# Kernel optimization log

Hardware: AMD Instinct MI355X
Metric: run time of the kernel (lower is better)

The kernel has to match this reference:

```python
import jax, jax.numpy as jnp
import numpy as np

OBS_DIM = 768; H = 128; W = 128
OBJ_DIM = 128; REL_DIM = 64; N_SLOTS = 32; ACT_DIM = 16; HID = 256
EPS = 1e-8; DT = 0.1; N_ITERS = 3
REND_IN = OBJ_DIM * N_SLOTS + REL_DIM * N_SLOTS * N_SLOTS  # 69632


def _ln(x, g, b):
    m = x.mean(-1, keepdims=True)
    v = ((x - m) ** 2).mean(-1, keepdims=True)
    return (x - m) / jnp.sqrt(v + 1e-5) * g + b


def setup_inputs() -> dict:
    key = jax.random.key(0)
    ks = iter(jax.random.split(key, 48))

    def w(shape):
        fan = shape[-2] if len(shape) > 1 else shape[0]
        return jax.random.normal(next(ks), shape, jnp.float32) / np.sqrt(fan)

    d = {}
    d['obs'] = jax.random.normal(next(ks), (1, H, W, OBS_DIM), jnp.float32)
    d['action'] = jax.random.normal(next(ks), (1, ACT_DIM), jnp.float32)
    d['slot_noise'] = jax.random.normal(next(ks), (1, N_SLOTS, OBJ_DIM), jnp.float32)
    d['slots_mu'] = jax.random.normal(next(ks), (1, 1, OBJ_DIM), jnp.float32)
    d['slots_log_sigma'] = jax.random.normal(next(ks), (1, 1, OBJ_DIM), jnp.float32) * 0.1 - 1.0
    d['ln_in_g'] = jnp.ones((OBS_DIM,)); d['ln_in_b'] = jnp.zeros((OBS_DIM,))
    d['ln_s_g'] = jnp.ones((OBJ_DIM,)); d['ln_s_b'] = jnp.zeros((OBJ_DIM,))
    d['ln_m_g'] = jnp.ones((OBJ_DIM,)); d['ln_m_b'] = jnp.zeros((OBJ_DIM,))
    d['Wq'] = w((OBJ_DIM, OBJ_DIM)); d['Wk'] = w((OBS_DIM, OBJ_DIM)); d['Wv'] = w((OBS_DIM, OBJ_DIM))
    d['mlp_w1'] = w((OBJ_DIM, 2 * OBJ_DIM)); d['mlp_b1'] = jnp.zeros((2 * OBJ_DIM,))
    d['mlp_w2'] = w((2 * OBJ_DIM, OBJ_DIM)); d['mlp_b2'] = jnp.zeros((OBJ_DIM,))
    d['prop_w1'] = w((OBJ_DIM, HID)); d['prop_b1'] = jnp.zeros((HID,))
    d['prop_w2'] = w((HID, OBJ_DIM)); d['prop_b2'] = jnp.zeros((OBJ_DIM,))
    d['rel_w1'] = w((2 * OBJ_DIM, 2 * REL_DIM)); d['rel_b1'] = jnp.zeros((2 * REL_DIM,))
    d['rel_w2'] = w((2 * REL_DIM, REL_DIM)); d['rel_b2'] = jnp.zeros((REL_DIM,))
    d['dyn_w1'] = w((OBJ_DIM + ACT_DIM, HID)); d['dyn_b1'] = jnp.zeros((HID,))
    d['dyn_w2'] = w((HID, HID)); d['dyn_b2'] = jnp.zeros((HID,))
    d['dyn_w3'] = w((HID, OBJ_DIM)); d['dyn_b3'] = jnp.zeros((OBJ_DIM,))
    d['gravity'] = jnp.array([0.0, -9.8, 0.0], jnp.float32)
    d['rend_w1'] = w((REND_IN, 2 * OBS_DIM)); d['rend_b1'] = jnp.zeros((2 * OBS_DIM,))
    d['rend_w2'] = w((2 * OBS_DIM, OBS_DIM)); d['rend_b2'] = jnp.zeros((OBS_DIM,))
    return d


def reference(obs, action, slot_noise, slots_mu, slots_log_sigma,
              ln_in_g, ln_in_b, ln_s_g, ln_s_b, ln_m_g, ln_m_b,
              Wq, Wk, Wv, mlp_w1, mlp_b1, mlp_w2, mlp_b2,
              prop_w1, prop_b1, prop_w2, prop_b2,
              rel_w1, rel_b1, rel_w2, rel_b2,
              dyn_w1, dyn_b1, dyn_w2, dyn_b2, dyn_w3, dyn_b3,
              gravity, rend_w1, rend_b1, rend_w2, rend_b2):
    B = obs.shape[0]
    # --- slot attention over flattened feature map ---
    x = obs.reshape(B, -1, OBS_DIM)                 # [B, HW, C]
    x = _ln(x, ln_in_g, ln_in_b)
    k = x @ Wk                                      # [B, HW, D]
    v = x @ Wv                                      # [B, HW, D]
    slots = slots_mu + jnp.exp(slots_log_sigma) * slot_noise  # [B, S, D]
    scale = OBJ_DIM ** -0.5
    for _ in range(N_ITERS):
        prev = slots
        q = _ln(slots, ln_s_g, ln_s_b) @ Wq
        logits = jnp.einsum('bsd,bnd->bsn', q, k) * scale
        attn = jax.nn.softmax(logits, axis=1)       # softmax over slots (dim=1)
        attn = attn / (attn.sum(-1, keepdims=True) + EPS)
        slots = prev + jnp.einsum('bsn,bnd->bsd', attn, v)
        h = _ln(slots, ln_m_g, ln_m_b)
        slots = slots + (jax.nn.relu(h @ mlp_w1 + mlp_b1) @ mlp_w2 + mlp_b2)
    # --- object property decoding ---
    objects = jax.nn.relu(slots @ prop_w1 + prop_b1) @ prop_w2 + prop_b2  # [B, S, D]
    # --- pairwise relation encoding (O(S^2)) ---
    S = N_SLOTS
    oi = jnp.broadcast_to(objects[:, :, None, :], (B, S, S, OBJ_DIM))
    oj = jnp.broadcast_to(objects[:, None, :, :], (B, S, S, OBJ_DIM))
    pairs = jnp.concatenate([oi, oj], -1)            # [B, S, S, 2D]
    relations = jax.nn.relu(pairs @ rel_w1 + rel_b1) @ rel_w2 + rel_b2  # [B, S, S, REL]
    # --- scene graph takes batch element 0 (as in torch source) ---
    obj0 = objects[0:1]                              # [1, S, D]
    rel0 = relations[0]                              # [S, S, REL]
    # --- physics engine ---
    a = jnp.broadcast_to(action[:, None, :], (1, S, ACT_DIM))
    inp = jnp.concatenate([obj0, a], -1)
    h = jax.nn.relu(inp @ dyn_w1 + dyn_b1)
    h = jax.nn.relu(h @ dyn_w2 + dyn_b2)
    delta = h @ dyn_w3 + dyn_b3                      # [1, S, D]
    delta = delta.at[:, :, :3].add(gravity * DT)
    next_objects = obj0 + delta * DT                 # [1, S, D]
    # --- render next observation ---
    feat = jnp.concatenate([next_objects.reshape(1, -1), rel0.reshape(1, -1)], -1)
    next_obs = jax.nn.relu(feat @ rend_w1 + rend_b1) @ rend_w2 + rend_b2  # [1, OBS_DIM]
    return next_obs
```

## Files before the change

kernel.cpp:

```cpp
#include <hip/hip_runtime.h>
#include <hip/hip_bf16.h>
#include <math.h>

#define NPIX    16384
#define OBSD    768
#define OBJ     128
#define NS      32
#define HIDD    256
#define RELD    64
#define ACTD    16
#define QSCALE  0.08838834764831845f
#define LNEPS   1e-5f
#define ATEPS   1e-8f
#define DTC     0.1f

#define OFF_STATS 0
#define OFF_KV    (OFF_STATS + NPIX*2)
#define OFF_SLOTS (OFF_KV + NPIX*256)
#define OFF_Q     (OFF_SLOTS + 4096)
#define OFF_H     (OFF_Q + 4096)
#define OFF_APART (OFF_H + 4096)
#define OFF_OBJ   (OFF_APART + 256*4128)
#define OFF_FEAT  (OFF_OBJ + 4096)
#define OFF_P1    (OFF_FEAT + 69632)
#define OFF_HREND (OFF_P1 + 1024*1536)
#define OFF_P3    (OFF_HREND + 1536)

__global__ __launch_bounds__(256) void k_stats_initq(
    const float* __restrict__ obs, float* __restrict__ stats,
    const float* __restrict__ mu, const float* __restrict__ lsig,
    const float* __restrict__ noise, float* __restrict__ slots,
    const float* __restrict__ Wq,
    const float* __restrict__ g, const float* __restrict__ b,
    float* __restrict__ qg)
{
    __shared__ float red[256];
    __shared__ float hh[128];
    int t = threadIdx.x;
    if (blockIdx.x < 4096) {
        int lane = t & 63;
        int w    = t >> 6;
        int row  = blockIdx.x * 4 + w;
        const float* o = obs + (size_t)row * OBSD;
        float s = 0.f, s2 = 0.f;
        #pragma unroll
        for (int i = 0; i < 12; ++i) { float v = o[lane + 64*i]; s += v; s2 += v*v; }
        #pragma unroll
        for (int off = 32; off > 0; off >>= 1) {
            s  += __shfl_down(s,  off);
            s2 += __shfl_down(s2, off);
        }
        if (lane == 0) {
            float m   = s  * (1.f/OBSD);
            float var = s2 * (1.f/OBSD) - m*m;
            stats[row*2]   = m;
            stats[row*2+1] = rsqrtf(var + LNEPS);
        }
        return;
    }
    int s = blockIdx.x - 4096;
    int d = t & 127, half = t >> 7;
    float x = 0.f;
    if (t < 128) {
        x = mu[t] + expf(lsig[t]) * noise[s*128 + t];
        slots[s*128 + t] = x;
    }
    red[t] = (t < 128) ? x : 0.f;
    __syncthreads();
    #pragma unroll
    for (int off = 128; off > 0; off >>= 1) { if (t < off) red[t] += red[t+off]; __syncthreads(); }
    float mean = red[0] * (1.f/128.f);
    __syncthreads();
    { float dx = (t < 128) ? (x - mean) : 0.f; red[t] = dx*dx; }
    __syncthreads();
    #pragma unroll
    for (int off = 128; off > 0; off >>= 1) { if (t < off) red[t] += red[t+off]; __syncthreads(); }
    float rstd = rsqrtf(red[0] * (1.f/128.f) + LNEPS);
    __syncthreads();
    if (t < 128) hh[t] = (x - mean) * rstd * g[t] + b[t];
    __syncthreads();
    float acc = 0.f;
    for (int c = half*64; c < half*64 + 64; ++c) acc = fmaf(hh[c], Wq[c*128 + d], acc);
    red[t] = acc;
    __syncthreads();
    if (t < 128) qg[s*128 + t] = red[t] + red[t+128];
}

#define STA 129
__global__ __launch_bounds__(256) void k_kv(
    const float* __restrict__ obs, const float* __restrict__ stats,
    const float* __restrict__ g, const float* __restrict__ b,
    const float* __restrict__ Wk, const float* __restrict__ Wv,
    float* __restrict__ kv)
{
    __shared__ float As[32*STA];
    __shared__ float Bs[32*128];
    __shared__ float sm[128], sr[128];
    int t  = threadIdx.x;
    int m0 = blockIdx.x * 128;
    int nsel = blockIdx.y;
    const float* W = nsel ? Wv : Wk;
    int tx = t & 15, ty = t >> 4;
    float acc[8][8];
    #pragma unroll
    for (int i = 0; i < 8; ++i) {
        #pragma unroll
        for (int j = 0; j < 8; ++j) acc[i][j] = 0.f;
    }
    if (t < 128) { sm[t] = stats[(m0+t)*2]; sr[t] = stats[(m0+t)*2+1]; }

    for (int ks = 0; ks < 24; ++ks) {
        int k0 = ks * 32;
        __syncthreads();
        #pragma unroll
        for (int r = 0; r < 16; ++r) {
            int id = t + 256*r;
            int m  = id >> 5, kk = id & 31;
            float val = obs[(size_t)(m0+m)*OBSD + k0 + kk];
            val = (val - sm[m]) * sr[m] * g[k0+kk] + b[k0+kk];
            As[kk*STA + m] = val;
        }
        #pragma unroll
        for (int r = 0; r < 16; ++r) {
            int id = t + 256*r;
            int kk = id >> 7, jj = id & 127;
            Bs[kk*128 + jj] = W[(size_t)(k0+kk)*128 + jj];
        }
        __syncthreads();
        #pragma unroll
        for (int kk = 0; kk < 32; ++kk) {
            float a8[8], b8[8];
            #pragma unroll
            for (int i = 0; i < 8; ++i) a8[i] = As[kk*STA + ty*8 + i];
            float4 u0 = *(const float4*)&Bs[kk*128 + tx*8];
            float4 u1 = *(const float4*)&Bs[kk*128 + tx*8 + 4];
            b8[0]=u0.x; b8[1]=u0.y; b8[2]=u0.z; b8[3]=u0.w;
            b8[4]=u1.x; b8[5]=u1.y; b8[6]=u1.z; b8[7]=u1.w;
            #pragma unroll
            for (int i = 0; i < 8; ++i) {
                #pragma unroll
                for (int j = 0; j < 8; ++j)
                    acc[i][j] = fmaf(a8[i], b8[j], acc[i][j]);
            }
        }
    }
    #pragma unroll
    for (int i = 0; i < 8; ++i) {
        size_t row = (size_t)(m0 + ty*8 + i);
        float4 o0 = make_float4(acc[i][0], acc[i][1], acc[i][2], acc[i][3]);
        float4 o1 = make_float4(acc[i][4], acc[i][5], acc[i][6], acc[i][7]);
        *(float4*)&kv[row*256 + nsel*128 + tx*8]     = o0;
        *(float4*)&kv[row*256 + nsel*128 + tx*8 + 4] = o1;
    }
}

#define STK 129
#define STQ 132
#define STT 36
__global__ __launch_bounds__(256) void k_attn(
    const float* __restrict__ kv, const float* __restrict__ qg,
    float* __restrict__ part)
{
    __shared__ float q_lds[NS*STQ];
    __shared__ float k_lds[64*STK];
    __shared__ float at[64*STT];
    int t   = threadIdx.x;
    int px0 = blockIdx.x * 64;
    #pragma unroll
    for (int r = 0; r < 16; ++r) {
        int id = t + 256*r;
        int s = id >> 7, d = id & 127;
        q_lds[s*STQ + d] = qg[id];
    }
    #pragma unroll
    for (int r = 0; r < 32; ++r) {
        int id = t + 256*r;
        int p = id >> 7, d = id & 127;
        k_lds[p*STK + d] = kv[(size_t)(px0+p)*256 + d];
    }
    __syncthreads();

    int wv = t >> 6, p = t & 63;
    float acc[8];
    #pragma unroll
    for (int u = 0; u < 8; ++u) acc[u] = 0.f;
    for (int dc = 0; dc < 4; ++dc) {
        float kr[32];
        #pragma unroll
        for (int d = 0; d < 32; ++d) kr[d] = k_lds[p*STK + dc*32 + d];
        #pragma unroll
        for (int u = 0; u < 8; ++u) {
            int s = u*4 + wv;
            const float* qp = &q_lds[s*STQ + dc*32];
            #pragma unroll
            for (int ii = 0; ii < 8; ++ii) {
                float4 q4 = *(const float4*)(qp + 4*ii);
                acc[u] = fmaf(q4.x, kr[4*ii+0], acc[u]);
                acc[u] = fmaf(q4.y, kr[4*ii+1], acc[u]);
                acc[u] = fmaf(q4.z, kr[4*ii+2], acc[u]);
                acc[u] = fmaf(q4.w, kr[4*ii+3], acc[u]);
            }
        }
    }
    #pragma unroll
    for (int u = 0; u < 8; ++u) at[p*STT + u*4 + wv] = acc[u] * QSCALE;
    __syncthreads();

    if (t < 64) {
        float mx = -1e30f;
        #pragma unroll
        for (int s = 0; s < NS; ++s) mx = fmaxf(mx, at[t*STT + s]);
        float smv = 0.f;
        #pragma unroll
        for (int s = 0; s < NS; ++s) { float e = expf(at[t*STT + s] - mx); at[t*STT + s] = e; smv += e; }
        float inv = 1.f / smv;
        #pragma unroll
        for (int s = 0; s < NS; ++s) at[t*STT + s] *= inv;
    }
    __syncthreads();

    int d = t & 127, sh = t >> 7;
    float u16[16];
    #pragma unroll
    for (int i = 0; i < 16; ++i) u16[i] = 0.f;
    const float* vbase = kv + (size_t)px0*256 + 128 + d;
    #pragma unroll 4
    for (int pp = 0; pp < 64; ++pp) {
        float vv = vbase[(size_t)pp*256];
        const float4* ap = (const float4*)&at[pp*STT + sh*16];
        #pragma unroll
        for (int gg = 0; gg < 4; ++gg) {
            float4 a4 = ap[gg];
            u16[4*gg+0] = fmaf(a4.x, vv, u16[4*gg+0]);
            u16[4*gg+1] = fmaf(a4.y, vv, u16[4*gg+1]);
            u16[4*gg+2] = fmaf(a4.z, vv, u16[4*gg+2]);
            u16[4*gg+3] = fmaf(a4.w, vv, u16[4*gg+3]);
        }
    }
    float* P = part + (size_t)blockIdx.x * 4128;
    #pragma unroll
    for (int g2 = 0; g2 < 16; ++g2) P[(sh*16 + g2)*128 + d] = u16[g2];
    if (t < 32) {
        float ss = 0.f;
        for (int pp = 0; pp < 64; ++pp) ss += at[pp*STT + t];
        P[4096 + t] = ss;
    }
}

__global__ __launch_bounds__(256) void k_umq(
    const float* __restrict__ part, float* __restrict__ slots,
    const float* __restrict__ gm, const float* __restrict__ bm,
    const float* __restrict__ w1, const float* __restrict__ b1,
    const float* __restrict__ w2, const float* __restrict__ b2,
    const float* __restrict__ gs, const float* __restrict__ bs,
    const float* __restrict__ Wq, float* __restrict__ qg,
    const float* __restrict__ pw1, const float* __restrict__ pb1,
    const float* __restrict__ pw2, const float* __restrict__ pb2,
    const float* __restrict__ action,
    const float* __restrict__ dw1, const float* __restrict__ db1,
    const float* __restrict__ dw2, const float* __restrict__ db2,
    const float* __restrict__ dw3, const float* __restrict__ db3,
    const float* __restrict__ gravity,
    float* __restrict__ objects, float* __restrict__ feat, int last)
{
    int s = blockIdx.x, t = threadIdx.x;
    int d = t & 127, half = t >> 7;
    __shared__ float red[256];
    __shared__ float ssred[2];
    __shared__ float xs[128], hm[128], hid[256];
    __shared__ float inp[144], h2[256];

    float u = 0.f, ss = 0.f;
    const float* P0 = part + (size_t)(half * 128) * 4128;
    for (int bb = 0; bb < 128; ++bb) {
        const float* P = P0 + (size_t)bb * 4128;
        u  += P[s*128 + d];
        ss += P[4096 + s];
    }
    red[t] = u;
    if (d == 0) ssred[half] = ss;
    __syncthreads();
    if (half == 0)
        xs[d] = slots[s*128 + d] + (red[d] + red[d+128]) / (ssred[0] + ssred[1] + ATEPS);
    __syncthreads();

    red[t] = (half == 0) ? xs[d] : 0.f;
    __syncthreads();
    #pragma unroll
    for (int off = 128; off > 0; off >>= 1) { if (t < off) red[t] += red[t+off]; __syncthreads(); }
    float mean = red[0] * (1.f/128.f);
    __syncthreads();
    { float dx = (half == 0) ? (xs[d] - mean) : 0.f; red[t] = dx*dx; }
    __syncthreads();
    #pragma unroll
    for (int off = 128; off > 0; off >>= 1) { if (t < off) red[t] += red[t+off]; __syncthreads(); }
    float rstd = rsqrtf(red[0] * (1.f/128.f) + LNEPS);
    __syncthreads();
    if (half == 0) hm[d] = (xs[d] - mean) * rstd * gm[d] + bm[d];
    __syncthreads();

    float a = b1[t];
    for (int c = 0; c < 128; ++c) a = fmaf(hm[c], w1[c*256 + t], a);
    hid[t] = fmaxf(a, 0.f);
    __syncthreads();
    if (half == 0) {
        float o = b2[d];
        for (int j = 0; j < 256; ++j) o = fmaf(hid[j], w2[j*128 + d], o);
        float xn = xs[d] + o;
        slots[s*128 + d] = xn;
        xs[d] = xn;
    }
    __syncthreads();

    if (!last) {
        red[t] = (half == 0) ? xs[d] : 0.f;
        __syncthreads();
        #pragma unroll
        for (int off = 128; off > 0; off >>= 1) { if (t < off) red[t] += red[t+off]; __syncthreads(); }
        float m2 = red[0] * (1.f/128.f);
        __syncthreads();
        { float dx = (half == 0) ? (xs[d] - m2) : 0.f; red[t] = dx*dx; }
        __syncthreads();
        #pragma unroll
        for (int off = 128; off > 0; off >>= 1) { if (t < off) red[t] += red[t+off]; __syncthreads(); }
        float r2 = rsqrtf(red[0] * (1.f/128.f) + LNEPS);
        __syncthreads();
        if (half == 0) hm[d] = (xs[d] - m2) * r2 * gs[d] + bs[d];
        __syncthreads();
        float acc = 0.f;
        for (int c = half*64; c < half*64 + 64; ++c) acc = fmaf(hm[c], Wq[c*128 + d], acc);
        red[t] = acc;
        __syncthreads();
        if (half == 0) qg[s*128 + d] = red[d] + red[d+128];
    } else {
        float a1 = pb1[t];
        for (int c = 0; c < 128; ++c) a1 = fmaf(xs[c], pw1[c*256 + t], a1);
        hid[t] = fmaxf(a1, 0.f);
        __syncthreads();
        if (t < 128) {
            float o = pb2[t];
            for (int j = 0; j < 256; ++j) o = fmaf(hid[j], pw2[j*128 + t], o);
            objects[s*128 + t] = o;
            inp[t] = o;
        } else if (t < 144) {
            inp[t] = action[t - 128];
        }
        __syncthreads();
        float a2 = db1[t];
        for (int c = 0; c < 144; ++c) a2 = fmaf(inp[c], dw1[c*256 + t], a2);
        hid[t] = fmaxf(a2, 0.f);
        __syncthreads();
        float a3 = db2[t];
        for (int c = 0; c < 256; ++c) a3 = fmaf(hid[c], dw2[c*256 + t], a3);
        h2[t] = fmaxf(a3, 0.f);
        __syncthreads();
        if (t < 128) {
            float dlt = db3[t];
            for (int c = 0; c < 256; ++c) dlt = fmaf(h2[c], dw3[c*128 + t], dlt);
            if (t < 3) dlt += gravity[t] * DTC;
            feat[s*128 + t] = inp[t] + dlt * DTC;
        }
    }
}

__global__ __launch_bounds__(128) void k_rel(
    const float* __restrict__ objects, const float* __restrict__ w1, const float* __restrict__ b1,
    const float* __restrict__ w2, const float* __restrict__ b2, float* __restrict__ rel_out)
{
    int pr = blockIdx.x; int i = pr >> 5, j = pr & 31; int t = threadIdx.x;
    __shared__ float pair[256], hid[128];
    pair[t]       = objects[i*128 + t];
    pair[128 + t] = objects[j*128 + t];
    __syncthreads();
    float a = b1[t];
    for (int c = 0; c < 256; ++c) a = fmaf(pair[c], w1[c*128 + t], a);
    hid[t] = fmaxf(a, 0.f);
    __syncthreads();
    if (t < 64) {
        float o = b2[t];
        for (int c = 0; c < 128; ++c) o = fmaf(hid[c], w2[c*64 + t], o);
        rel_out[(size_t)pr*64 + t] = o;
    }
}

__global__ __launch_bounds__(384) void k_rend1(
    const float* __restrict__ feat, const float* __restrict__ w1, float* __restrict__ p1)
{
    int b = blockIdx.x, t = threadIdx.x;
    float4 acc = make_float4(0.f, 0.f, 0.f, 0.f);
    int i0 = b * 68;
    #pragma unroll 4
    for (int r = 0; r < 68; ++r) {
        int i = i0 + r;
        float f = feat[i];
        float4 w = *(const float4*)(w1 + (size_t)i * 1536 + 4*t);
        acc.x = fmaf(f, w.x, acc.x);
        acc.y = fmaf(f, w.y, acc.y);
        acc.z = fmaf(f, w.z, acc.z);
        acc.w = fmaf(f, w.w, acc.w);
    }
    *(float4*)(p1 + (size_t)b * 1536 + 4*t) = acc;
}

__global__ __launch_bounds__(256) void k_rend23(
    const float* __restrict__ p1, const float* __restrict__ b1,
    const float* __restrict__ w2, float* __restrict__ p3)
{
    int bj = blockIdx.x, t = threadIdx.x;
    int j0 = bj * 32;
    int tj = t & 31, tr = t >> 5;
    __shared__ float red2[256];
    __shared__ float hh[32];
    float part = 0.f;
    const float* P = p1 + (size_t)tr * 1536 + j0 + tj;
    #pragma unroll 8
    for (int r = 0; r < 128; ++r) part += P[(size_t)r * 8 * 1536];
    red2[t] = part;
    __syncthreads();
    if (t < 32) {
        float a = b1[j0 + t];
        #pragma unroll
        for (int g = 0; g < 8; ++g) a += red2[g*32 + t];
        hh[t] = fmaxf(a, 0.f);
    }
    __syncthreads();
    float a0 = 0.f, a1 = 0.f, a2 = 0.f;
    #pragma unroll
    for (int j = 0; j < 32; ++j) {
        float hj = hh[j];
        const float* w = w2 + (size_t)(j0 + j) * 768;
        a0 = fmaf(hj, w[t],       a0);
        a1 = fmaf(hj, w[t + 256], a1);
        a2 = fmaf(hj, w[t + 512], a2);
    }
    p3[(size_t)bj*768 + t]       = a0;
    p3[(size_t)bj*768 + t + 256] = a1;
    p3[(size_t)bj*768 + t + 512] = a2;
}

__global__ __launch_bounds__(256) void k_rend4(
    const float* __restrict__ p3, const float* __restrict__ b2, float* __restrict__ out)
{
    int m = blockIdx.x * 256 + threadIdx.x;
    float a = b2[m];
    #pragma unroll
    for (int bj = 0; bj < 48; ++bj) a += p3[(size_t)bj*768 + m];
    out[m] = a;
}

extern "C" void kernel_launch(void* const* d_in, const int* in_sizes, int n_in,
                              void* d_out, int out_size, void* d_ws, size_t ws_size,
                              hipStream_t stream) {
    (void)in_sizes; (void)n_in; (void)out_size; (void)ws_size;
    const float* obs      = (const float*)d_in[0];
    const float* action   = (const float*)d_in[1];
    const float* noise    = (const float*)d_in[2];
    const float* mu       = (const float*)d_in[3];
    const float* lsig     = (const float*)d_in[4];
    const float* ln_in_g  = (const float*)d_in[5];
    const float* ln_in_b  = (const float*)d_in[6];
    const float* ln_s_g   = (const float*)d_in[7];
    const float* ln_s_b   = (const float*)d_in[8];
    const float* ln_m_g   = (const float*)d_in[9];
    const float* ln_m_b   = (const float*)d_in[10];
    const float* Wq       = (const float*)d_in[11];
    const float* Wk       = (const float*)d_in[12];
    const float* Wv       = (const float*)d_in[13];
    const float* mlp_w1   = (const float*)d_in[14];
    const float* mlp_b1   = (const float*)d_in[15];
    const float* mlp_w2   = (const float*)d_in[16];
    const float* mlp_b2   = (const float*)d_in[17];
    const float* prop_w1  = (const float*)d_in[18];
    const float* prop_b1  = (const float*)d_in[19];
    const float* prop_w2  = (const float*)d_in[20];
    const float* prop_b2  = (const float*)d_in[21];
    const float* rel_w1   = (const float*)d_in[22];
    const float* rel_b1   = (const float*)d_in[23];
    const float* rel_w2   = (const float*)d_in[24];
    const float* rel_b2   = (const float*)d_in[25];
    const float* dyn_w1   = (const float*)d_in[26];
    const float* dyn_b1   = (const float*)d_in[27];
    const float* dyn_w2   = (const float*)d_in[28];
    const float* dyn_b2   = (const float*)d_in[29];
    const float* dyn_w3   = (const float*)d_in[30];
    const float* dyn_b3   = (const float*)d_in[31];
    const float* gravity  = (const float*)d_in[32];
    const float* rend_w1  = (const float*)d_in[33];
    const float* rend_b1  = (const float*)d_in[34];
    const float* rend_w2  = (const float*)d_in[35];
    const float* rend_b2  = (const float*)d_in[36];
    float* out = (float*)d_out;

    float* w      = (float*)d_ws;
    float* stats  = w + OFF_STATS;
    float* kv     = w + OFF_KV;
    float* slots  = w + OFF_SLOTS;
    float* qg     = w + OFF_Q;
    float* apart  = w + OFF_APART;
    float* objs   = w + OFF_OBJ;
    float* feat   = w + OFF_FEAT;
    float* relout = feat + 4096;
    float* p1     = w + OFF_P1;
    float* p3     = w + OFF_P3;

    k_stats_initq<<<4128, 256, 0, stream>>>(obs, stats, mu, lsig, noise, slots,
                                            Wq, ln_s_g, ln_s_b, qg);
    k_kv<<<dim3(128, 2), 256, 0, stream>>>(obs, stats, ln_in_g, ln_in_b, Wk, Wv, kv);

    for (int it = 0; it < 3; ++it) {
        k_attn<<<256, 256, 0, stream>>>(kv, qg, apart);
        k_umq<<<32, 256, 0, stream>>>(apart, slots, ln_m_g, ln_m_b,
                                      mlp_w1, mlp_b1, mlp_w2, mlp_b2,
                                      ln_s_g, ln_s_b, Wq, qg,
                                      prop_w1, prop_b1, prop_w2, prop_b2,
                                      action, dyn_w1, dyn_b1, dyn_w2, dyn_b2,
                                      dyn_w3, dyn_b3, gravity,
                                      objs, feat, (it == 2) ? 1 : 0);
    }

    k_rel<<<1024, 128, 0, stream>>>(objs, rel_w1, rel_b1, rel_w2, rel_b2, relout);

    k_rend1<<<1024, 384, 0, stream>>>(feat, rend_w1, p1);
    k_rend23<<<48, 256, 0, stream>>>(p1, rend_b1, rend_w2, p3);
    k_rend4<<<3, 256, 0, stream>>>(p3, rend_b2, out);
}
```

Baseline: 985.2 us.

## Fuse slot-attention iterations and relation MLP into persistent kernel with grid barrier

Replaces the six alternating attention/update kernel launches and the relation kernel with one persistent 256-block kernel. Phases are separated by a software sense-reversing grid barrier built on atomics. The goal is to remove launch gaps and tail effects between the small dependent kernels. In exchange it needs all 256 blocks co-resident to avoid deadlock, idles most blocks during the 32-block update phase, and pays atomic spin-wait costs at each barrier.

```diff
diff --git a/kernel.cpp b/kernel.cpp
--- a/kernel.cpp
+++ b/kernel.cpp
@@ -25,6 +25,7 @@
 #define OFF_P1    (OFF_FEAT + 69632)
 #define OFF_HREND (OFF_P1 + 1024*1536)
 #define OFF_P3    (OFF_HREND + 1536)
+#define OFF_BAR   (OFF_P3 + 48*768)
 
 __global__ __launch_bounds__(256) void k_stats_initq(
     const float* __restrict__ obs, float* __restrict__ stats,
@@ -32,7 +33,7 @@
     const float* __restrict__ noise, float* __restrict__ slots,
     const float* __restrict__ Wq,
     const float* __restrict__ g, const float* __restrict__ b,
-    float* __restrict__ qg)
+    float* __restrict__ qg, int* __restrict__ bar)
 {
     __shared__ float red[256];
     __shared__ float hh[128];
@@ -59,6 +60,7 @@
         return;
     }
     int s = blockIdx.x - 4096;
+    if (s == 0 && t < 2) bar[t] = 0;
     int d = t & 127, half = t >> 7;
     float x = 0.f;
     if (t < 128) {
@@ -154,232 +156,255 @@
     }
 }
 
+__device__ __forceinline__ void gbar(int* cnt, int* sense, int nblk, int want)
+{
+    __syncthreads();
+    if (threadIdx.x == 0) {
+        __threadfence();
+        int prev = atomicAdd(cnt, 1);
+        if (prev == nblk - 1) {
+            atomicExch(cnt, 0);
+            __threadfence();
+            atomicExch(sense, want);
+        } else {
+            while (atomicAdd(sense, 0) != want)
+                __builtin_amdgcn_s_sleep(2);
+            __threadfence();
+        }
+    }
+    __syncthreads();
+}
+
 #define STK 129
 #define STQ 132
 #define STT 36
-__global__ __launch_bounds__(256) void k_attn(
-    const float* __restrict__ kv, const float* __restrict__ qg,
-    float* __restrict__ part)
-{
-    __shared__ float q_lds[NS*STQ];
-    __shared__ float k_lds[64*STK];
-    __shared__ float at[64*STT];
+
+struct SLArgs {
+    const float* kv;
+    const float* gs; const float* bs; const float* Wq;
+    const float* gm; const float* bm;
+    const float* w1; const float* b1; const float* w2; const float* b2;
+    const float* pw1; const float* pb1; const float* pw2; const float* pb2;
+    const float* action;
+    const float* dw1; const float* db1; const float* dw2; const float* db2;
+    const float* dw3; const float* db3; const float* gravity;
+    const float* rw1; const float* rb1; const float* rw2; const float* rb2;
+    float* slots; float* qg; float* part; float* objects; float* feat; float* relout;
+    int* bcnt; int* bsen;
+};
+
+__global__ __launch_bounds__(256) void k_mega(SLArgs a)
+{
+    __shared__ union {
+        struct { float q[NS*STQ]; float k[64*STK]; float at[64*STT]; } A;
+        struct { float red[256]; float ssred[2]; float xs[128]; float hm[128];
+                 float hid[256]; float inp[144]; float h2[256]; } U;
+        struct { float pair[2][256]; float hid[2][128]; } R;
+    } sm;
     int t   = threadIdx.x;
-    int px0 = blockIdx.x * 64;
-    #pragma unroll
-    for (int r = 0; r < 16; ++r) {
-        int id = t + 256*r;
-        int s = id >> 7, d = id & 127;
-        q_lds[s*STQ + d] = qg[id];
-    }
-    #pragma unroll
-    for (int r = 0; r < 32; ++r) {
-        int id = t + 256*r;
-        int p = id >> 7, d = id & 127;
-        k_lds[p*STK + d] = kv[(size_t)(px0+p)*256 + d];
-    }
-    __syncthreads();
-
-    int wv = t >> 6, p = t & 63;
-    float acc[8];
-    #pragma unroll
-    for (int u = 0; u < 8; ++u) acc[u] = 0.f;
-    for (int dc = 0; dc < 4; ++dc) {
-        float kr[32];
-        #pragma unroll
-        for (int d = 0; d < 32; ++d) kr[d] = k_lds[p*STK + dc*32 + d];
-        #pragma unroll
-        for (int u = 0; u < 8; ++u) {
-            int s = u*4 + wv;
-            const float* qp = &q_lds[s*STQ + dc*32];
-            #pragma unroll
-            for (int ii = 0; ii < 8; ++ii) {
-                float4 q4 = *(const float4*)(qp + 4*ii);
-                acc[u] = fmaf(q4.x, kr[4*ii+0], acc[u]);
-                acc[u] = fmaf(q4.y, kr[4*ii+1], acc[u]);
-                acc[u] = fmaf(q4.z, kr[4*ii+2], acc[u]);
-                acc[u] = fmaf(q4.w, kr[4*ii+3], acc[u]);
-            }
-        }
-    }
-    #pragma unroll
-    for (int u = 0; u < 8; ++u) at[p*STT + u*4 + wv] = acc[u] * QSCALE;
-    __syncthreads();
-
-    if (t < 64) {
-        float mx = -1e30f;
-        #pragma unroll
-        for (int s = 0; s < NS; ++s) mx = fmaxf(mx, at[t*STT + s]);
-        float smv = 0.f;
-        #pragma unroll
-        for (int s = 0; s < NS; ++s) { float e = expf(at[t*STT + s] - mx); at[t*STT + s] = e; smv += e; }
-        float inv = 1.f / smv;
-        #pragma unroll
-        for (int s = 0; s < NS; ++s) at[t*STT + s] *= inv;
-    }
-    __syncthreads();
-
-    int d = t & 127, sh = t >> 7;
-    float u16[16];
-    #pragma unroll
-    for (int i = 0; i < 16; ++i) u16[i] = 0.f;
-    const float* vbase = kv + (size_t)px0*256 + 128 + d;
-    #pragma unroll 4
-    for (int pp = 0; pp < 64; ++pp) {
-        float vv = vbase[(size_t)pp*256];
-        const float4* ap = (const float4*)&at[pp*STT + sh*16];
-        #pragma unroll
-        for (int gg = 0; gg < 4; ++gg) {
-            float4 a4 = ap[gg];
-            u16[4*gg+0] = fmaf(a4.x, vv, u16[4*gg+0]);
-            u16[4*gg+1] = fmaf(a4.y, vv, u16[4*gg+1]);
-            u16[4*gg+2] = fmaf(a4.z, vv, u16[4*gg+2]);
-            u16[4*gg+3] = fmaf(a4.w, vv, u16[4*gg+3]);
-        }
-    }
-    float* P = part + (size_t)blockIdx.x * 4128;
-    #pragma unroll
-    for (int g2 = 0; g2 < 16; ++g2) P[(sh*16 + g2)*128 + d] = u16[g2];
-    if (t < 32) {
-        float ss = 0.f;
-        for (int pp = 0; pp < 64; ++pp) ss += at[pp*STT + t];
-        P[4096 + t] = ss;
-    }
-}
-
-__global__ __launch_bounds__(256) void k_umq(
-    const float* __restrict__ part, float* __restrict__ slots,
-    const float* __restrict__ gm, const float* __restrict__ bm,
-    const float* __restrict__ w1, const float* __restrict__ b1,
-    const float* __restrict__ w2, const float* __restrict__ b2,
-    const float* __restrict__ gs, const float* __restrict__ bs,
-    const float* __restrict__ Wq, float* __restrict__ qg,
-    const float* __restrict__ pw1, const float* __restrict__ pb1,
-    const float* __restrict__ pw2, const float* __restrict__ pb2,
-    const float* __restrict__ action,
-    const float* __restrict__ dw1, const float* __restrict__ db1,
-    const float* __restrict__ dw2, const float* __restrict__ db2,
-    const float* __restrict__ dw3, const float* __restrict__ db3,
-    const float* __restrict__ gravity,
-    float* __restrict__ objects, float* __restrict__ feat, int last)
-{
-    int s = blockIdx.x, t = threadIdx.x;
+    int blk = blockIdx.x;
     int d = t & 127, half = t >> 7;
-    __shared__ float red[256];
-    __shared__ float ssred[2];
-    __shared__ float xs[128], hm[128], hid[256];
-    __shared__ float inp[144], h2[256];
-
-    float u = 0.f, ss = 0.f;
-    const float* P0 = part + (size_t)(half * 128) * 4128;
-    for (int bb = 0; bb < 128; ++bb) {
-        const float* P = P0 + (size_t)bb * 4128;
-        u  += P[s*128 + d];
-        ss += P[4096 + s];
-    }
-    red[t] = u;
-    if (d == 0) ssred[half] = ss;
-    __syncthreads();
-    if (half == 0)
-        xs[d] = slots[s*128 + d] + (red[d] + red[d+128]) / (ssred[0] + ssred[1] + ATEPS);
-    __syncthreads();
-
-    red[t] = (half == 0) ? xs[d] : 0.f;
-    __syncthreads();
-    #pragma unroll
-    for (int off = 128; off > 0; off >>= 1) { if (t < off) red[t] += red[t+off]; __syncthreads(); }
-    float mean = red[0] * (1.f/128.f);
-    __syncthreads();
-    { float dx = (half == 0) ? (xs[d] - mean) : 0.f; red[t] = dx*dx; }
-    __syncthreads();
-    #pragma unroll
-    for (int off = 128; off > 0; off >>= 1) { if (t < off) red[t] += red[t+off]; __syncthreads(); }
-    float rstd = rsqrtf(red[0] * (1.f/128.f) + LNEPS);
-    __syncthreads();
-    if (half == 0) hm[d] = (xs[d] - mean) * rstd * gm[d] + bm[d];
-    __syncthreads();
-
-    float a = b1[t];
-    for (int c = 0; c < 128; ++c) a = fmaf(hm[c], w1[c*256 + t], a);
-    hid[t] = fmaxf(a, 0.f);
-    __syncthreads();
-    if (half == 0) {
-        float o = b2[d];
-        for (int j = 0; j < 256; ++j) o = fmaf(hid[j], w2[j*128 + d], o);
-        float xn = xs[d] + o;
-        slots[s*128 + d] = xn;
-        xs[d] = xn;
-    }
-    __syncthreads();
-
-    if (!last) {
-        red[t] = (half == 0) ? xs[d] : 0.f;
+    int ls = 0;
+
+    for (int it = 0; it < 3; ++it) {
+        {
+            int px0 = blk * 64;
+            __syncthreads();
+            #pragma unroll
+            for (int r = 0; r < 16; ++r) {
+                int id = t + 256*r;
+                int s2 = id >> 7, dd = id & 127;
+                sm.A.q[s2*STQ + dd] = a.qg[id];
+            }
+            #pragma unroll
+            for (int r = 0; r < 32; ++r) {
+                int id = t + 256*r;
+                int p = id >> 7, dd = id & 127;
+                sm.A.k[p*STK + dd] = a.kv[(size_t)(px0+p)*256 + dd];
+            }
+            __syncthreads();
+
+            int wv = t >> 6, p = t & 63;
+            float acc[8];
+            #pragma unroll
+            for (int u = 0; u < 8; ++u) acc[u] = 0.f;
+            for (int dc = 0; dc < 4; ++dc) {
+                float kr[32];
+                #pragma unroll
+                for (int dd = 0; dd < 32; ++dd) kr[dd] = sm.A.k[p*STK + dc*32 + dd];
+                #pragma unroll
+                for (int u = 0; u < 8; ++u) {
+                    int s2 = u*4 + wv;
+                    const float* qp = &sm.A.q[s2*STQ + dc*32];
+                    #pragma unroll
+                    for (int ii = 0; ii < 8; ++ii) {
+                        float4 q4 = *(const float4*)(qp + 4*ii);
+                        acc[u] = fmaf(q4.x, kr[4*ii+0], acc[u]);
+                        acc[u] = fmaf(q4.y, kr[4*ii+1], acc[u]);
+                        acc[u] = fmaf(q4.z, kr[4*ii+2], acc[u]);
+                        acc[u] = fmaf(q4.w, kr[4*ii+3], acc[u]);
+                    }
+                }
+            }
+            #pragma unroll
+            for (int u = 0; u < 8; ++u) sm.A.at[p*STT + u*4 + wv] = acc[u] * QSCALE;
+            __syncthreads();
+
+            if (t < 64) {
+                float mx = -1e30f;
+                #pragma unroll
+                for (int s2 = 0; s2 < NS; ++s2) mx = fmaxf(mx, sm.A.at[t*STT + s2]);
+                float smv = 0.f;
+                #pragma unroll
+                for (int s2 = 0; s2 < NS; ++s2) { float e = expf(sm.A.at[t*STT + s2] - mx); sm.A.at[t*STT + s2] = e; smv += e; }
+                float inv = 1.f / smv;
+                #pragma unroll
+                for (int s2 = 0; s2 < NS; ++s2) sm.A.at[t*STT + s2] *= inv;
+            }
+            __syncthreads();
+
+            int sh = t >> 7;
+            float u16[16];
+            #pragma unroll
+            for (int i = 0; i < 16; ++i) u16[i] = 0.f;
+            const float* vbase = a.kv + (size_t)px0*256 + 128 + d;
+            #pragma unroll 4
+            for (int pp = 0; pp < 64; ++pp) {
+                float vv = vbase[(size_t)pp*256];
+                const float4* ap = (const float4*)&sm.A.at[pp*STT + sh*16];
+                #pragma unroll
+                for (int gg = 0; gg < 4; ++gg) {
+                    float4 a4 = ap[gg];
+                    u16[4*gg+0] = fmaf(a4.x, vv, u16[4*gg+0]);
+                    u16[4*gg+1] = fmaf(a4.y, vv, u16[4*gg+1]);
+                    u16[4*gg+2] = fmaf(a4.z, vv, u16[4*gg+2]);
+                    u16[4*gg+3] = fmaf(a4.w, vv, u16[4*gg+3]);
+                }
+            }
+            float* P = a.part + (size_t)blk * 4128;
+            #pragma unroll
+            for (int g2 = 0; g2 < 16; ++g2) P[(sh*16 + g2)*128 + d] = u16[g2];
+            if (t < 32) {
+                float ss = 0.f;
+                for (int pp = 0; pp < 64; ++pp) ss += sm.A.at[pp*STT + t];
+                P[4096 + t] = ss;
+            }
+        }
+        ls ^= 1; gbar(a.bcnt, a.bsen, 256, ls);
+
+        if (blk < NS) {
+            int s = blk;
+            float u = 0.f, ss = 0.f;
+            const float* P0 = a.part + (size_t)(half * 128) * 4128;
+            for (int bb = 0; bb < 128; ++bb) {
+                const float* P = P0 + (size_t)bb * 4128;
+                u  += P[s*128 + d];
+                ss += P[4096 + s];
+            }
+            sm.U.red[t] = u;
+            if (d == 0) sm.U.ssred[half] = ss;
+            __syncthreads();
+            if (half == 0)
+                sm.U.xs[d] = a.slots[s*128 + d] + (sm.U.red[d] + sm.U.red[d+128]) / (sm.U.ssred[0] + sm.U.ssred[1] + ATEPS);
+            __syncthreads();
+
+            sm.U.red[t] = (half == 0) ? sm.U.xs[d] : 0.f;
+            __syncthreads();
+            #pragma unroll
+            for (int off = 128; off > 0; off >>= 1) { if (t < off) sm.U.red[t] += sm.U.red[t+off]; __syncthreads(); }
+            float mean = sm.U.red[0] * (1.f/128.f);
+            __syncthreads();
+            { float dx = (half == 0) ? (sm.U.xs[d] - mean) : 0.f; sm.U.red[t] = dx*dx; }
+            __syncthreads();
+            #pragma unroll
+            for (int off = 128; off > 0; off >>= 1) { if (t < off) sm.U.red[t] += sm.U.red[t+off]; __syncthreads(); }
+            float rstd = rsqrtf(sm.U.red[0] * (1.f/128.f) + LNEPS);
+            __syncthreads();
+            if (half == 0) sm.U.hm[d] = (sm.U.xs[d] - mean) * rstd * a.gm[d] + a.bm[d];
+            __syncthreads();
+
+            float aa = a.b1[t];
+            for (int c = 0; c < 128; ++c) aa = fmaf(sm.U.hm[c], a.w1[c*256 + t], aa);
+            sm.U.hid[t] = fmaxf(aa, 0.f);
+            __syncthreads();
+            if (half == 0) {
+                float o = a.b2[d];
+                for (int j = 0; j < 256; ++j) o = fmaf(sm.U.hid[j], a.w2[j*128 + d], o);
+                float xn = sm.U.xs[d] + o;
+                a.slots[s*128 + d] = xn;
+                sm.U.xs[d] = xn;
+            }
+            __syncthreads();
+
+            if (it < 2) {
+                sm.U.red[t] = (half == 0) ? sm.U.xs[d] : 0.f;
+                __syncthreads();
+                #pragma unroll
+                for (int off = 128; off > 0; off >>= 1) { if (t < off) sm.U.red[t] += sm.U.red[t+off]; __syncthreads(); }
+                float m2 = sm.U.red[0] * (1.f/128.f);
+                __syncthreads();
+                { float dx = (half == 0) ? (sm.U.xs[d] - m2) : 0.f; sm.U.red[t] = dx*dx; }
+                __syncthreads();
+                #pragma unroll
+                for (int off = 128; off > 0; off >>= 1) { if (t < off) sm.U.red[t] += sm.U.red[t+off]; __syncthreads(); }
+                float r2 = rsqrtf(sm.U.red[0] * (1.f/128.f) + LNEPS);
+                __syncthreads();
+                if (half == 0) sm.U.hm[d] = (sm.U.xs[d] - m2) * r2 * a.gs[d] + a.bs[d];
+                __syncthreads();
+                float acc = 0.f;
+                for (int c = half*64; c < half*64 + 64; ++c) acc = fmaf(sm.U.hm[c], a.Wq[c*128 + d], acc);
+                sm.U.red[t] = acc;
+                __syncthreads();
+                if (half == 0) a.qg[s*128 + d] = sm.U.red[d] + sm.U.red[d+128];
+            } else {
+                float a1 = a.pb1[t];
+                for (int c = 0; c < 128; ++c) a1 = fmaf(sm.U.xs[c], a.pw1[c*256 + t], a1);
+                sm.U.hid[t] = fmaxf(a1, 0.f);
+                __syncthreads();
+                if (t < 128) {
+                    float o = a.pb2[t];
+                    for (int j = 0; j < 256; ++j) o = fmaf(sm.U.hid[j], a.pw2[j*128 + t], o);
+                    a.objects[s*128 + t] = o;
+                    sm.U.inp[t] = o;
+                } else if (t < 144) {
+                    sm.U.inp[t] = a.action[t - 128];
+                }
+                __syncthreads();
+                float a2 = a.db1[t];
+                for (int c = 0; c < 144; ++c) a2 = fmaf(sm.U.inp[c], a.dw1[c*256 + t], a2);
+                sm.U.hid[t] = fmaxf(a2, 0.f);
+                __syncthreads();
+                float a3 = a.db2[t];
+                for (int c = 0; c < 256; ++c) a3 = fmaf(sm.U.hid[c], a.dw2[c*256 + t], a3);
+                sm.U.h2[t] = fmaxf(a3, 0.f);
+                __syncthreads();
+                if (t < 128) {
+                    float dlt = a.db3[t];
+                    for (int c = 0; c < 256; ++c) dlt = fmaf(sm.U.h2[c], a.dw3[c*128 + t], dlt);
+                    if (t < 3) dlt += a.gravity[t] * DTC;
+                    a.feat[s*128 + t] = sm.U.inp[t] + dlt * DTC;
+                }
+            }
+        }
+        ls ^= 1; gbar(a.bcnt, a.bsen, 256, ls);
+    }
+
+    for (int rep = 0; rep < 2; ++rep) {
+        int pr = blk*4 + rep*2 + half;
+        int i = pr >> 5, j = pr & 31;
         __syncthreads();
-        #pragma unroll
-        for (int off = 128; off > 0; off >>= 1) { if (t < off) red[t] += red[t+off]; __syncthreads(); }
-        float m2 = red[0] * (1.f/128.f);
+        sm.R.pair[half][d]       = a.objects[i*128 + d];
+        sm.R.pair[half][d + 128] = a.objects[j*128 + d];
         __syncthreads();
-        { float dx = (half == 0) ? (xs[d] - m2) : 0.f; red[t] = dx*dx; }
+        float aa = a.rb1[d];
+        for (int c = 0; c < 256; ++c) aa = fmaf(sm.R.pair[half][c], a.rw1[c*128 + d], aa);
+        sm.R.hid[half][d] = fmaxf(aa, 0.f);
         __syncthreads();
-        #pragma unroll
-        for (int off = 128; off > 0; off >>= 1) { if (t < off) red[t] += red[t+off]; __syncthreads(); }
-        float r2 = rsqrtf(red[0] * (1.f/128.f) + LNEPS);
-        __syncthreads();
-        if (half == 0) hm[d] = (xs[d] - m2) * r2 * gs[d] + bs[d];
-        __syncthreads();
-        float acc = 0.f;
-        for (int c = half*64; c < half*64 + 64; ++c) acc = fmaf(hm[c], Wq[c*128 + d], acc);
-        red[t] = acc;
-        __syncthreads();
-        if (half == 0) qg[s*128 + d] = red[d] + red[d+128];
-    } else {
-        float a1 = pb1[t];
-        for (int c = 0; c < 128; ++c) a1 = fmaf(xs[c], pw1[c*256 + t], a1);
-        hid[t] = fmaxf(a1, 0.f);
-        __syncthreads();
-        if (t < 128) {
-            float o = pb2[t];
-            for (int j = 0; j < 256; ++j) o = fmaf(hid[j], pw2[j*128 + t], o);
-            objects[s*128 + t] = o;
-            inp[t] = o;
-        } else if (t < 144) {
-            inp[t] = action[t - 128];
-        }
-        __syncthreads();
-        float a2 = db1[t];
-        for (int c = 0; c < 144; ++c) a2 = fmaf(inp[c], dw1[c*256 + t], a2);
-        hid[t] = fmaxf(a2, 0.f);
-        __syncthreads();
-        float a3 = db2[t];
-        for (int c = 0; c < 256; ++c) a3 = fmaf(hid[c], dw2[c*256 + t], a3);
-        h2[t] = fmaxf(a3, 0.f);
-        __syncthreads();
-        if (t < 128) {
-            float dlt = db3[t];
-            for (int c = 0; c < 256; ++c) dlt = fmaf(h2[c], dw3[c*128 + t], dlt);
-            if (t < 3) dlt += gravity[t] * DTC;
-            feat[s*128 + t] = inp[t] + dlt * DTC;
-        }
-    }
-}
-
-__global__ __launch_bounds__(128) void k_rel(
-    const float* __restrict__ objects, const float* __restrict__ w1, const float* __restrict__ b1,
-    const float* __restrict__ w2, const float* __restrict__ b2, float* __restrict__ rel_out)
-{
-    int pr = blockIdx.x; int i = pr >> 5, j = pr & 31; int t = threadIdx.x;
-    __shared__ float pair[256], hid[128];
-    pair[t]       = objects[i*128 + t];
-    pair[128 + t] = objects[j*128 + t];
-    __syncthreads();
-    float a = b1[t];
-    for (int c = 0; c < 256; ++c) a = fmaf(pair[c], w1[c*128 + t], a);
-    hid[t] = fmaxf(a, 0.f);
-    __syncthreads();
-    if (t < 64) {
-        float o = b2[t];
-        for (int c = 0; c < 128; ++c) o = fmaf(hid[c], w2[c*64 + t], o);
-        rel_out[(size_t)pr*64 + t] = o;
+        if (d < 64) {
+            float o = a.rb2[d];
+            for (int c = 0; c < 128; ++c) o = fmaf(sm.R.hid[half][c], a.rw2[c*64 + d], o);
+            a.relout[(size_t)pr*64 + d] = o;
+        }
     }
 }
 
@@ -502,23 +527,26 @@
     float* relout = feat + 4096;
     float* p1     = w + OFF_P1;
     float* p3     = w + OFF_P3;
+    int*   bar    = (int*)(w + OFF_BAR);
 
     k_stats_initq<<<4128, 256, 0, stream>>>(obs, stats, mu, lsig, noise, slots,
-                                            Wq, ln_s_g, ln_s_b, qg);
+                                            Wq, ln_s_g, ln_s_b, qg, bar);
     k_kv<<<dim3(128, 2), 256, 0, stream>>>(obs, stats, ln_in_g, ln_in_b, Wk, Wv, kv);
 
-    for (int it = 0; it < 3; ++it) {
-        k_attn<<<256, 256, 0, stream>>>(kv, qg, apart);
-        k_umq<<<32, 256, 0, stream>>>(apart, slots, ln_m_g, ln_m_b,
-                                      mlp_w1, mlp_b1, mlp_w2, mlp_b2,
-                                      ln_s_g, ln_s_b, Wq, qg,
-                                      prop_w1, prop_b1, prop_w2, prop_b2,
-                                      action, dyn_w1, dyn_b1, dyn_w2, dyn_b2,
-                                      dyn_w3, dyn_b3, gravity,
-                                      objs, feat, (it == 2) ? 1 : 0);
-    }
-
-    k_rel<<<1024, 128, 0, stream>>>(objs, rel_w1, rel_b1, rel_w2, rel_b2, relout);
+    SLArgs sa;
+    sa.kv = kv;
+    sa.gs = ln_s_g; sa.bs = ln_s_b; sa.Wq = Wq;
+    sa.gm = ln_m_g; sa.bm = ln_m_b;
+    sa.w1 = mlp_w1; sa.b1 = mlp_b1; sa.w2 = mlp_w2; sa.b2 = mlp_b2;
+    sa.pw1 = prop_w1; sa.pb1 = prop_b1; sa.pw2 = prop_w2; sa.pb2 = prop_b2;
+    sa.action = action;
+    sa.dw1 = dyn_w1; sa.db1 = dyn_b1; sa.dw2 = dyn_w2; sa.db2 = dyn_b2;
+    sa.dw3 = dyn_w3; sa.db3 = dyn_b3; sa.gravity = gravity;
+    sa.rw1 = rel_w1; sa.rb1 = rel_b1; sa.rw2 = rel_w2; sa.rb2 = rel_b2;
+    sa.slots = slots; sa.qg = qg; sa.part = apart;
+    sa.objects = objs; sa.feat = feat; sa.relout = relout;
+    sa.bcnt = bar; sa.bsen = bar + 1;
+    k_mega<<<256, 256, 0, stream>>>(sa);
 
     k_rend1<<<1024, 384, 0, stream>>>(feat, rend_w1, p1);
     k_rend23<<<48, 256, 0, stream>>>(p1, rend_b1, rend_w2, p3);
```

New measurement: 1.556 ms. +57.9%, slower.

## Fuse LayerNorm stats and slot init into KV GEMM; fuse relation MLP into render

Applied to the files above, without the earlier changes.

Removes the separate stats/initq kernel. Each KV GEMM block now computes the LayerNorm mean and rstd for its own 128 rows, and the first 32 blocks also do slot initialization and the first Wq projection. It also removes the k_rel kernel: render-layer-1 blocks that cover the relation part of the feature vector compute the needed pair relations on the fly. This saves launches and the global round trips for stats and relations. In exchange, each row's stats are computed twice (once per Wk/Wv block), and some render blocks do a serial relation MLP before their GEMV.

```diff
diff --git a/kernel.cpp b/kernel.cpp
--- a/kernel.cpp
+++ b/kernel.cpp
@@ -26,88 +26,87 @@
 #define OFF_HREND (OFF_P1 + 1024*1536)
 #define OFF_P3    (OFF_HREND + 1536)
 
-__global__ __launch_bounds__(256) void k_stats_initq(
-    const float* __restrict__ obs, float* __restrict__ stats,
+#define STA 129
+__global__ __launch_bounds__(256) void k_kv(
+    const float* __restrict__ obs,
+    const float* __restrict__ g, const float* __restrict__ b,
+    const float* __restrict__ Wk, const float* __restrict__ Wv,
+    float* __restrict__ kv,
     const float* __restrict__ mu, const float* __restrict__ lsig,
     const float* __restrict__ noise, float* __restrict__ slots,
     const float* __restrict__ Wq,
-    const float* __restrict__ g, const float* __restrict__ b,
+    const float* __restrict__ gs, const float* __restrict__ bs,
     float* __restrict__ qg)
-{
-    __shared__ float red[256];
-    __shared__ float hh[128];
-    int t = threadIdx.x;
-    if (blockIdx.x < 4096) {
-        int lane = t & 63;
-        int w    = t >> 6;
-        int row  = blockIdx.x * 4 + w;
-        const float* o = obs + (size_t)row * OBSD;
-        float s = 0.f, s2 = 0.f;
-        #pragma unroll
-        for (int i = 0; i < 12; ++i) { float v = o[lane + 64*i]; s += v; s2 += v*v; }
-        #pragma unroll
-        for (int off = 32; off > 0; off >>= 1) {
-            s  += __shfl_down(s,  off);
-            s2 += __shfl_down(s2, off);
-        }
-        if (lane == 0) {
-            float m   = s  * (1.f/OBSD);
-            float var = s2 * (1.f/OBSD) - m*m;
-            stats[row*2]   = m;
-            stats[row*2+1] = rsqrtf(var + LNEPS);
-        }
-        return;
-    }
-    int s = blockIdx.x - 4096;
-    int d = t & 127, half = t >> 7;
-    float x = 0.f;
-    if (t < 128) {
-        x = mu[t] + expf(lsig[t]) * noise[s*128 + t];
-        slots[s*128 + t] = x;
-    }
-    red[t] = (t < 128) ? x : 0.f;
-    __syncthreads();
-    #pragma unroll
-    for (int off = 128; off > 0; off >>= 1) { if (t < off) red[t] += red[t+off]; __syncthreads(); }
-    float mean = red[0] * (1.f/128.f);
-    __syncthreads();
-    { float dx = (t < 128) ? (x - mean) : 0.f; red[t] = dx*dx; }
-    __syncthreads();
-    #pragma unroll
-    for (int off = 128; off > 0; off >>= 1) { if (t < off) red[t] += red[t+off]; __syncthreads(); }
-    float rstd = rsqrtf(red[0] * (1.f/128.f) + LNEPS);
-    __syncthreads();
-    if (t < 128) hh[t] = (x - mean) * rstd * g[t] + b[t];
-    __syncthreads();
-    float acc = 0.f;
-    for (int c = half*64; c < half*64 + 64; ++c) acc = fmaf(hh[c], Wq[c*128 + d], acc);
-    red[t] = acc;
-    __syncthreads();
-    if (t < 128) qg[s*128 + t] = red[t] + red[t+128];
-}
-
-#define STA 129
-__global__ __launch_bounds__(256) void k_kv(
-    const float* __restrict__ obs, const float* __restrict__ stats,
-    const float* __restrict__ g, const float* __restrict__ b,
-    const float* __restrict__ Wk, const float* __restrict__ Wv,
-    float* __restrict__ kv)
 {
     __shared__ float As[32*STA];
     __shared__ float Bs[32*128];
     __shared__ float sm[128], sr[128];
+    __shared__ float red[256];
+    __shared__ float hh[128];
     int t  = threadIdx.x;
     int m0 = blockIdx.x * 128;
     int nsel = blockIdx.y;
     const float* W = nsel ? Wv : Wk;
     int tx = t & 15, ty = t >> 4;
+
+    if (nsel == 0 && blockIdx.x < NS) {
+        int s = blockIdx.x;
+        int d = t & 127, half = t >> 7;
+        float x = 0.f;
+        if (t < 128) {
+            x = mu[t] + expf(lsig[t]) * noise[s*128 + t];
+            slots[s*128 + t] = x;
+        }
+        red[t] = (t < 128) ? x : 0.f;
+        __syncthreads();
+        #pragma unroll
+        for (int off = 128; off > 0; off >>= 1) { if (t < off) red[t] += red[t+off]; __syncthreads(); }
+        float mean = red[0] * (1.f/128.f);
+        __syncthreads();
+        { float dx = (t < 128) ? (x - mean) : 0.f; red[t] = dx*dx; }
+        __syncthreads();
+        #pragma unroll
+        for (int off = 128; off > 0; off >>= 1) { if (t < off) red[t] += red[t+off]; __syncthreads(); }
+        float rstd = rsqrtf(red[0] * (1.f/128.f) + LNEPS);
+        __syncthreads();
+        if (t < 128) hh[t] = (x - mean) * rstd * gs[t] + bs[t];
+        __syncthreads();
+        float acc = 0.f;
+        for (int c = half*64; c < half*64 + 64; ++c) acc = fmaf(hh[c], Wq[c*128 + d], acc);
+        red[t] = acc;
+        __syncthreads();
+        if (t < 128) qg[s*128 + t] = red[t] + red[t+128];
+        __syncthreads();
+    }
+
+    {
+        int lane = t & 63, wvi = t >> 6;
+        for (int rr = 0; rr < 32; ++rr) {
+            int row = wvi * 32 + rr;
+            const float* o = obs + (size_t)(m0 + row) * OBSD;
+            float s1 = 0.f, s2 = 0.f;
+            #pragma unroll
+            for (int i = 0; i < 12; ++i) { float v = o[lane + 64*i]; s1 += v; s2 += v*v; }
+            #pragma unroll
+            for (int off = 32; off > 0; off >>= 1) {
+                s1 += __shfl_down(s1, off);
+                s2 += __shfl_down(s2, off);
+            }
+            if (lane == 0) {
+                float m   = s1 * (1.f/OBSD);
+                float var = s2 * (1.f/OBSD) - m*m;
+                sm[row] = m;
+                sr[row] = rsqrtf(var + LNEPS);
+            }
+        }
+    }
+
     float acc[8][8];
     #pragma unroll
     for (int i = 0; i < 8; ++i) {
         #pragma unroll
         for (int j = 0; j < 8; ++j) acc[i][j] = 0.f;
     }
-    if (t < 128) { sm[t] = stats[(m0+t)*2]; sr[t] = stats[(m0+t)*2+1]; }
 
     for (int ks = 0; ks < 24; ++ks) {
         int k0 = ks * 32;
@@ -363,43 +362,62 @@
     }
 }
 
-__global__ __launch_bounds__(128) void k_rel(
-    const float* __restrict__ objects, const float* __restrict__ w1, const float* __restrict__ b1,
-    const float* __restrict__ w2, const float* __restrict__ b2, float* __restrict__ rel_out)
+__global__ __launch_bounds__(384) void k_rend1(
+    const float* __restrict__ feat, const float* __restrict__ objects,
+    const float* __restrict__ rw1, const float* __restrict__ rb1,
+    const float* __restrict__ rw2, const float* __restrict__ rb2,
+    const float* __restrict__ w1, float* __restrict__ p1)
 {
-    int pr = blockIdx.x; int i = pr >> 5, j = pr & 31; int t = threadIdx.x;
-    __shared__ float pair[256], hid[128];
-    pair[t]       = objects[i*128 + t];
-    pair[128 + t] = objects[j*128 + t];
-    __syncthreads();
-    float a = b1[t];
-    for (int c = 0; c < 256; ++c) a = fmaf(pair[c], w1[c*128 + t], a);
-    hid[t] = fmaxf(a, 0.f);
-    __syncthreads();
-    if (t < 64) {
-        float o = b2[t];
-        for (int c = 0; c < 128; ++c) o = fmaf(hid[c], w2[c*64 + t], o);
-        rel_out[(size_t)pr*64 + t] = o;
-    }
-}
-
-__global__ __launch_bounds__(384) void k_rend1(
-    const float* __restrict__ feat, const float* __restrict__ w1, float* __restrict__ p1)
-{
-    int b = blockIdx.x, t = threadIdx.x;
+    __shared__ float fl[68];
+    __shared__ float pairb[256];
+    __shared__ float hidb[128];
+    __shared__ float prout[3][64];
+    int bq = blockIdx.x, t = threadIdx.x;
+    int i0 = bq * 68;
+    int q_hi = i0 + 67 - 4096;
+    if (q_hi >= 0) {
+        int q_lo = i0 - 4096;
+        int pr_lo = (q_lo > 0 ? q_lo : 0) >> 6;
+        int pr_hi = q_hi >> 6;
+        for (int pr = pr_lo; pr <= pr_hi; ++pr) {
+            int ii = pr >> 5, jj = pr & 31;
+            if (t < 128)      pairb[t] = objects[ii*128 + t];
+            else if (t < 256) pairb[t] = objects[jj*128 + (t - 128)];
+            __syncthreads();
+            if (t < 128) {
+                float a = rb1[t];
+                for (int c = 0; c < 256; ++c) a = fmaf(pairb[c], rw1[c*128 + t], a);
+                hidb[t] = fmaxf(a, 0.f);
+            }
+            __syncthreads();
+            if (t < 64) {
+                float o = rb2[t];
+                for (int c = 0; c < 128; ++c) o = fmaf(hidb[c], rw2[c*64 + t], o);
+                prout[pr - pr_lo][t] = o;
+            }
+            __syncthreads();
+        }
+        if (t < 68) {
+            int i = i0 + t;
+            if (i < 4096) fl[t] = feat[i];
+            else { int q = i - 4096; fl[t] = prout[(q >> 6) - pr_lo][q & 63]; }
+        }
+    } else {
+        if (t < 68) fl[t] = feat[i0 + t];
+    }
+    __syncthreads();
+
     float4 acc = make_float4(0.f, 0.f, 0.f, 0.f);
-    int i0 = b * 68;
     #pragma unroll 4
     for (int r = 0; r < 68; ++r) {
-        int i = i0 + r;
-        float f = feat[i];
-        float4 w = *(const float4*)(w1 + (size_t)i * 1536 + 4*t);
+        float f = fl[r];
+        float4 w = *(const float4*)(w1 + (size_t)(i0 + r) * 1536 + 4*t);
         acc.x = fmaf(f, w.x, acc.x);
         acc.y = fmaf(f, w.y, acc.y);
         acc.z = fmaf(f, w.z, acc.z);
         acc.w = fmaf(f, w.w, acc.w);
     }
-    *(float4*)(p1 + (size_t)b * 1536 + 4*t) = acc;
+    *(float4*)(p1 + (size_t)bq * 1536 + 4*t) = acc;
 }
 
 __global__ __launch_bounds__(256) void k_rend23(
@@ -492,20 +510,18 @@
     float* out = (float*)d_out;
 
     float* w      = (float*)d_ws;
-    float* stats  = w + OFF_STATS;
     float* kv     = w + OFF_KV;
     float* slots  = w + OFF_SLOTS;
     float* qg     = w + OFF_Q;
     float* apart  = w + OFF_APART;
     float* objs   = w + OFF_OBJ;
     float* feat   = w + OFF_FEAT;
-    float* relout = feat + 4096;
     float* p1     = w + OFF_P1;
     float* p3     = w + OFF_P3;
 
-    k_stats_initq<<<4128, 256, 0, stream>>>(obs, stats, mu, lsig, noise, slots,
-                                            Wq, ln_s_g, ln_s_b, qg);
-    k_kv<<<dim3(128, 2), 256, 0, stream>>>(obs, stats, ln_in_g, ln_in_b, Wk, Wv, kv);
+    k_kv<<<dim3(128, 2), 256, 0, stream>>>(obs, ln_in_g, ln_in_b, Wk, Wv, kv,
+                                           mu, lsig, noise, slots,
+                                           Wq, ln_s_g, ln_s_b, qg);
 
     for (int it = 0; it < 3; ++it) {
         k_attn<<<256, 256, 0, stream>>>(kv, qg, apart);
@@ -518,9 +534,8 @@
                                       objs, feat, (it == 2) ? 1 : 0);
     }
 
-    k_rel<<<1024, 128, 0, stream>>>(objs, rel_w1, rel_b1, rel_w2, rel_b2, relout);
-
-    k_rend1<<<1024, 384, 0, stream>>>(feat, rend_w1, p1);
+    k_rend1<<<1024, 384, 0, stream>>>(feat, objs, rel_w1, rel_b1, rel_w2, rel_b2,
+                                      rend_w1, p1);
     k_rend23<<<48, 256, 0, stream>>>(p1, rend_b1, rend_w2, p3);
     k_rend4<<<3, 256, 0, stream>>>(p3, rend_b2, out);
 }
```

After: 994.8 us. Within noise of the previous version (+1.0%).
